# Kernel optimization log

Hardware: AMD Instinct MI355X
Metric: run time of the kernel (lower is better)

The kernel has to match this reference:

```python
import jax, jax.numpy as jnp
import numpy as np

SR = 16000
N_FFT = 1024
HOP = 256
WIN = 1024
N_MELS = 80
EPS = 1e-8
DRY_W, RIR_W = 3.0, 1.0
TIME_W, FREQ_W, MEL_W = 1.0, 0.5, 0.3
CONSIST_W, RIR_REG_W = 0.2, 0.1


def _hann(n):
    # torch.hann_window(periodic=True)
    return (0.5 - 0.5 * jnp.cos(2.0 * jnp.pi * jnp.arange(n) / n)).astype(jnp.float32)


def _stft(x):
    """torchaudio.transforms.Spectrogram(power=None, normalized=True) equivalent.
    x: [..., T] -> complex [..., n_freqs, n_frames]"""
    shp = x.shape
    T = shp[-1]
    xf = x.reshape(-1, T)
    pad = N_FFT // 2
    xp = jnp.pad(xf, ((0, 0), (pad, pad)), mode='reflect')  # center=True
    n_frames = 1 + T // HOP
    idx = jnp.arange(n_frames)[:, None] * HOP + jnp.arange(N_FFT)[None, :]
    win = _hann(WIN)
    frames = xp[:, idx] * win[None, None, :]              # [N, frames, n_fft]
    spec = jnp.fft.rfft(frames, axis=-1)                  # [N, frames, freqs]
    spec = spec / jnp.sqrt(jnp.sum(win ** 2))             # normalized='window'
    return spec.reshape(shp[:-1] + (n_frames, N_FFT // 2 + 1)).swapaxes(-1, -2)


def _mel_fb():
    # torchaudio melscale_fbanks, htk scale, norm=None, f_min=0, f_max=sr/2
    n_freqs = N_FFT // 2 + 1
    all_freqs = np.linspace(0.0, SR / 2.0, n_freqs)
    hz2mel = lambda f: 2595.0 * np.log10(1.0 + f / 700.0)
    mel2hz = lambda m: 700.0 * (10.0 ** (m / 2595.0) - 1.0)
    m_pts = np.linspace(hz2mel(0.0), hz2mel(SR / 2.0), N_MELS + 2)
    f_pts = mel2hz(m_pts)
    f_diff = f_pts[1:] - f_pts[:-1]
    slopes = f_pts[None, :] - all_freqs[:, None]
    down = -slopes[:, :-2] / f_diff[:-1]
    up = slopes[:, 2:] / f_diff[1:]
    fb = np.maximum(0.0, np.minimum(down, up))
    return jnp.asarray(fb, jnp.float32)  # [n_freqs, n_mels]

_FB = _mel_fb()


def _l1(a, b):
    return jnp.mean(jnp.abs(a - b))


def _freq_loss(pred, target):
    ps, ts = _stft(pred), _stft(target)
    mag_loss = _l1(jnp.abs(ps), jnp.abs(ts))
    dphi = jnp.angle(ps) - jnp.angle(ts)
    # cosine sim of unit [cos, sin] vectors == cos(delta phase)
    phase_loss = 1.0 - jnp.mean(jnp.cos(dphi))
    return mag_loss + 0.1 * phase_loss


def _mel_loss(pred, target):
    pm = jnp.einsum('...ft,fm->...mt', jnp.abs(_stft(pred)) ** 2, _FB)
    tm = jnp.einsum('...ft,fm->...mt', jnp.abs(_stft(target)) ** 2, _FB)
    return _l1(jnp.log(pm + EPS), jnp.log(tm + EPS))


def _consistency_loss(pred_dry, pred_rir, mix):
    # full linear convolution along time, truncated to first T samples
    T = pred_dry.shape[-1]
    n = 2 * T
    D = jnp.fft.rfft(pred_dry, n=n, axis=-1)
    R = jnp.fft.rfft(pred_rir, n=n, axis=-1)
    rec = jnp.fft.irfft(D * R, n=n, axis=-1)[..., :T]
    return _l1(rec, mix[..., :T])


def _rir_reg_loss(pred_rir):
    T = pred_rir.shape[-1]
    sparsity = jnp.mean(jnp.abs(pred_rir))
    seg = T // 4
    decay = 0.0
    for i in range(3):
        e1 = jnp.mean(pred_rir[:, :, i * seg:(i + 1) * seg] ** 2)
        e2 = jnp.mean(pred_rir[:, :, (i + 1) * seg:(i + 2) * seg] ** 2)
        decay = decay + jax.nn.relu(e2 - 0.8 * e1)
    return sparsity + decay


def setup_inputs() -> dict:
    key = jax.random.key(0)
    ks = jax.random.split(key, 5)
    shape = (32, 2, 64000)
    names = ['pred_dry', 'pred_rir', 'target_dry', 'target_rir', 'mix']
    return {n: jax.random.normal(k, shape, dtype=jnp.float32) for n, k in zip(names, ks)}


def reference(pred_dry, pred_rir, target_dry, target_rir, mix):
    dry_time = _l1(pred_dry, target_dry)
    dry_freq = _freq_loss(pred_dry, target_dry)
    dry_mel = _mel_loss(pred_dry, target_dry)
    total_dry = TIME_W * dry_time + FREQ_W * dry_freq + MEL_W * dry_mel

    rir_time = _l1(pred_rir, target_rir)
    rir_reg = _rir_reg_loss(pred_rir)
    total_rir = rir_time + RIR_REG_W * rir_reg

    consist = _consistency_loss(pred_dry, pred_rir, mix)
    total = DRY_W * total_dry + RIR_W * total_rir + CONSIST_W * consist
    return total
```

## Files before the change

### kernel.cpp

```cpp
#include <hip/hip_runtime.h>
#include <math.h>

#define ROWS 64
#define TLEN 64000
#define NFR 251
#define NMELS 80
#define NFB 131072
#define PI2F 6.28318530717958647692f
#define PI_F 3.14159265358979323846f

__device__ double g_part[64][12];

__device__ constexpr int DR[16] = {0,4,8,12,1,5,9,13,2,6,10,14,3,7,11,15};
__device__ constexpr int RM[16] = {0,3,2,1,15,14,13,12,11,10,9,8,7,6,5,4};

__device__ inline int dr4(int i){ return ((i & 3) << 2) | (i >> 2); }
__device__ inline int SW(int k){ return k + (k >> 5); }

__device__ inline void atomAddD(double* p, double v){
  __hip_atomic_fetch_add(p, v, __ATOMIC_RELAXED, __HIP_MEMORY_SCOPE_AGENT);
}
__device__ inline int brev6(int x){ return (int)((unsigned)__brev((unsigned)x) >> 26); }
__device__ inline float2 cmul(float2 a, float2 b){
  return make_float2(a.x*b.x - a.y*b.y, a.x*b.y + a.y*b.x);
}
__device__ inline float wred(float v){
#pragma unroll
  for (int o = 32; o > 0; o >>= 1) v += __shfl_down(v, o, 64);
  return v;
}

__device__ inline void wave_fence(){
  asm volatile("s_waitcnt lgkmcnt(0)" ::: "memory");
}

template<int S, int N>
__device__ inline void fft64_lanes(float2* v, int l){
  float2 W[5];
#pragma unroll
  for (int si = 0; si < 5; ++si){
    int d = 32 >> si;
    float a = (float)S * PI_F * (float)(l & (d-1)) * (1.0f/(float)d);
    float sn, cs; __sincosf(a, &sn, &cs);
    W[si] = make_float2(cs, sn);
  }
#pragma unroll
  for (int si = 0; si < 6; ++si){
    int d = 32 >> si;
    bool hi = (l & d) != 0;
#pragma unroll
    for (int rr = 0; rr < N; ++rr){
      float2 x = v[rr];
      float tx = __shfl_xor(x.x, d, 64);
      float ty = __shfl_xor(x.y, d, 64);
      float sx = x.x + tx, sy = x.y + ty;
      float dx = tx - x.x, dy = ty - x.y;
      float rx, ry;
      if (si < 5){ rx = dx*W[si].x - dy*W[si].y; ry = dx*W[si].y + dy*W[si].x; }
      else       { rx = dx; ry = dy; }
      v[rr].x = hi ? rx : sx;
      v[rr].y = hi ? ry : sy;
    }
  }
}

template<int S>
__device__ inline void fft16_reg(float2* v){
  const float Sf = (float)S;
  const float C1 = 0.9238795325112867f, S1 = 0.3826834323650898f, C2 = 0.7071067811865476f;
  const float2 W1[4] = {{1.f,0.f},{C1,Sf*S1},{C2,Sf*C2},{S1,Sf*C1}};
  const float2 W2[4] = {{1.f,0.f},{C2,Sf*C2},{0.f,Sf},{-C2,Sf*C2}};
  const float2 W3[4] = {{1.f,0.f},{S1,Sf*C1},{-C2,Sf*C2},{-C1,-Sf*S1}};
#pragma unroll
  for (int j = 0; j < 4; ++j){
    float2 x0=v[j], x1=v[j+4], x2=v[j+8], x3=v[j+12];
    float2 t0={x0.x+x2.x, x0.y+x2.y}, t1={x0.x-x2.x, x0.y-x2.y};
    float2 t2={x1.x+x3.x, x1.y+x3.y}, t3={x1.x-x3.x, x1.y-x3.y};
    float2 y0={t0.x+t2.x, t0.y+t2.y};
    float2 y2={t0.x-t2.x, t0.y-t2.y};
    float2 y1={t1.x - Sf*t3.y, t1.y + Sf*t3.x};
    float2 y3={t1.x + Sf*t3.y, t1.y - Sf*t3.x};
    v[j]=y0; v[j+4]=cmul(y1,W1[j]); v[j+8]=cmul(y2,W2[j]); v[j+12]=cmul(y3,W3[j]);
  }
#pragma unroll
  for (int b = 0; b < 4; ++b){
    float2 x0=v[4*b], x1=v[4*b+1], x2=v[4*b+2], x3=v[4*b+3];
    float2 t0={x0.x+x2.x, x0.y+x2.y}, t1={x0.x-x2.x, x0.y-x2.y};
    float2 t2={x1.x+x3.x, x1.y+x3.y}, t3={x1.x-x3.x, x1.y-x3.y};
    v[4*b]   = make_float2(t0.x+t2.x, t0.y+t2.y);
    v[4*b+2] = make_float2(t0.x-t2.x, t0.y-t2.y);
    v[4*b+1] = make_float2(t1.x - Sf*t3.y, t1.y + Sf*t3.x);
    v[4*b+3] = make_float2(t1.x + Sf*t3.y, t1.y - Sf*t3.x);
  }
}

template<int S>
__device__ inline void fft128_wave(float2* v, int l){
  float2 a = {v[0].x+v[1].x, v[0].y+v[1].y};
  float2 b = {v[0].x-v[1].x, v[0].y-v[1].y};
  float ang = (float)S * PI_F * (float)l * (1.0f/64.0f);
  float sn, cs; __sincosf(ang, &sn, &cs);
  v[0] = a; v[1] = cmul(b, make_float2(cs, sn));
  fft64_lanes<S,2>(v, l);
}

template<int S>
__device__ inline void fft8p(float2* y){
  const float Sf = (float)S;
  const float C2 = 0.7071067811865476f;
  float2 t0={y[0].x+y[4].x, y[0].y+y[4].y};
  float2 t1={y[1].x+y[5].x, y[1].y+y[5].y};
  float2 t2={y[2].x+y[6].x, y[2].y+y[6].y};
  float2 t3={y[3].x+y[7].x, y[3].y+y[7].y};
  float2 u0={y[0].x-y[4].x, y[0].y-y[4].y};
  float2 u1={y[1].x-y[5].x, y[1].y-y[5].y};
  float2 u2={y[2].x-y[6].x, y[2].y-y[6].y};
  float2 u3={y[3].x-y[7].x, y[3].y-y[7].y};
  { float x=u1.x, yy=u1.y; u1.x = C2*(x - Sf*yy); u1.y = C2*(Sf*x + yy); }
  { float x=u2.x, yy=u2.y; u2.x = -Sf*yy;         u2.y = Sf*x; }
  { float x=u3.x, yy=u3.y; u3.x = -C2*(x + Sf*yy); u3.y = C2*(Sf*x - yy); }
  {
    float2 e0={t0.x+t2.x,t0.y+t2.y}, e1={t0.x-t2.x,t0.y-t2.y};
    float2 o0={t1.x+t3.x,t1.y+t3.y}, o1={t1.x-t3.x,t1.y-t3.y};
    y[0]=make_float2(e0.x+o0.x, e0.y+o0.y);
    y[4]=make_float2(e0.x-o0.x, e0.y-o0.y);
    y[2]=make_float2(e1.x - Sf*o1.y, e1.y + Sf*o1.x);
    y[6]=make_float2(e1.x + Sf*o1.y, e1.y - Sf*o1.x);
  }
  {
    float2 e0={u0.x+u2.x,u0.y+u2.y}, e1={u0.x-u2.x,u0.y-u2.y};
    float2 o0={u1.x+u3.x,u1.y+u3.y}, o1={u1.x-u3.x,u1.y-u3.y};
    y[1]=make_float2(e0.x+o0.x, e0.y+o0.y);
    y[5]=make_float2(e0.x-o0.x, e0.y-o0.y);
    y[3]=make_float2(e1.x - Sf*o1.y, e1.y + Sf*o1.x);
    y[7]=make_float2(e1.x + Sf*o1.y, e1.y - Sf*o1.x);
  }
}

template<int S>
__device__ inline void fft64_lds(float2* v, int l, float2* scr){
  int s = l >> 3, a = l & 7;
  int sw = (s & 1);
#pragma unroll
  for (int h = 0; h < 2; ++h){
    float2* vh = v + 8*h;
#pragma unroll
    for (int r = 0; r < 8; ++r) scr[r*64 + l] = vh[r];
    wave_fence();
    float2 y[8];
#pragma unroll
    for (int j = 0; j < 8; ++j)
      y[j] = scr[s*64 + a + 8*((j + s) & 7)];
    fft8p<S>(y);
    {
      float ang = (float)S * PI2F * (float)l * (1.0f/64.0f);
      float sn, cs; __sincosf(ang, &sn, &cs);
      float2 b1 = make_float2(cs, sn), cur = b1;
#pragma unroll
      for (int c = 1; c < 8; ++c){
        y[c] = cmul(y[c], cur);
        if (c < 7) cur = cmul(cur, b1);
      }
    }
    wave_fence();
#pragma unroll
    for (int c = 0; c < 8; ++c)
      scr[s*64 + a + 8*(c ^ sw)] = y[c];
    wave_fence();
    float2 z[8];
#pragma unroll
    for (int j = 0; j < 8; ++j)
      z[j] = scr[s*64 + ((j + s) & 7) + 8*(a ^ sw)];
    fft8p<S>(z);
    {
      float ang2 = (float)S * PI2F * (float)s * 0.125f;
      float sn2, cs2; __sincosf(ang2, &sn2, &cs2);
      float2 b2 = make_float2(cs2, sn2), cur = b2;
#pragma unroll
      for (int d = 1; d < 8; ++d){
        z[d] = cmul(z[d], cur);
        if (d < 7) cur = cmul(cur, b2);
      }
    }
    wave_fence();
#pragma unroll
    for (int d = 0; d < 8; ++d)
      scr[s*64 + a + 8*(d ^ sw)] = z[d];
    wave_fence();
#pragma unroll
    for (int r = 0; r < 8; ++r)
      vh[r] = scr[r*64 + (l ^ ((r & 1) << 3))];
    wave_fence();
  }
}

template<int S>
__device__ inline void fft1024_lds(float2* v, int l, float2* scr){
  fft16_reg<S>(v);
  float a = (float)S * PI2F * (float)l * (1.0f/1024.0f);
  float sn, cs; __sincosf(a, &sn, &cs);
  float2 T = make_float2(cs, sn);
  float2 cur = T;
#pragma unroll
  for (int k2 = 1; k2 < 16; ++k2){
    v[DR[k2]] = cmul(v[DR[k2]], cur);
    if (k2 < 15) cur = cmul(cur, T);
  }
  fft64_lds<S>(v, l, scr);
}

__device__ inline void r4p(float2* v, int i0, int i1, int i2, int i3){
  float2 x0=v[i0], x1=v[i1], x2=v[i2], x3=v[i3];
  float2 t0={x0.x+x2.x, x0.y+x2.y}, t1={x0.x-x2.x, x0.y-x2.y};
  float2 t2={x1.x+x3.x, x1.y+x3.y}, t3={x1.x-x3.x, x1.y-x3.y};
  v[i0] = make_float2(t0.x+t2.x, t0.y+t2.y);
  v[i2] = make_float2(t0.x-t2.x, t0.y-t2.y);
  v[i1] = make_float2(t1.x - t3.y, t1.y + t3.x);
  v[i3] = make_float2(t1.x + t3.y, t1.y - t3.x);
}

__device__ inline void ifft16_reg(float2* v){
#pragma unroll
  for (int b = 0; b < 4; ++b) r4p(v, 4*b, 4*b+1, 4*b+2, 4*b+3);
  const float C1 = 0.9238795325112867f, S1 = 0.3826834323650898f, C2 = 0.7071067811865476f;
  const float2 W1[4] = {{1.f,0.f},{C1,S1},{C2,C2},{S1,C1}};
  const float2 W2[4] = {{1.f,0.f},{C2,C2},{0.f,1.f},{-C2,C2}};
  const float2 W3[4] = {{1.f,0.f},{S1,C1},{-C2,C2},{-C1,-S1}};
#pragma unroll
  for (int j = 1; j < 4; ++j){
    v[j+4]  = cmul(v[j+4],  W1[j]);
    v[j+8]  = cmul(v[j+8],  W2[j]);
    v[j+12] = cmul(v[j+12], W3[j]);
  }
#pragma unroll
  for (int j = 0; j < 4; ++j) r4p(v, j, j+4, j+8, j+12);
}

__device__ inline void ifft1024_lds(float2* v, int l, float2* scr){
  fft64_lds<1>(v, l, scr);
  float a = PI2F * (float)l * (1.0f/1024.0f);
  float sn, cs; __sincosf(a, &sn, &cs);
  float2 T = make_float2(cs, sn);
  float2 cur = T;
#pragma unroll
  for (int k2 = 1; k2 < 16; ++k2){
    v[DR[k2]] = cmul(v[DR[k2]], cur);
    if (k2 < 15) cur = cmul(cur, T);
  }
  ifft16_reg(v);
}

template<int N>
__device__ inline void ifft64_lanes(float2* v, int l){
  float2 W[5];
#pragma unroll
  for (int si = 0; si < 5; ++si){
    int d = 32 >> si;
    float a = PI_F * (float)(l & (d-1)) * (1.0f/(float)d);
    float sn, cs; __sincosf(a, &sn, &cs);
    W[si] = make_float2(cs, sn);
  }
#pragma unroll
  for (int si = 5; si >= 0; --si){
    int d = 32 >> si;
    bool hi = (l & d) != 0;
#pragma unroll
    for (int rr = 0; rr < N; ++rr){
      float2 x = v[rr];
      float2 xp = x;
      if (si < 5 && hi) xp = cmul(x, W[si]);
      float tx = __shfl_xor(xp.x, d, 64);
      float ty = __shfl_xor(xp.y, d, 64);
      v[rr].x = hi ? (tx - xp.x) : (xp.x + tx);
      v[rr].y = hi ? (ty - xp.y) : (xp.y + ty);
    }
  }
}

__device__ inline void ifft128_wave(float2* v, int l){
  ifft64_lanes<2>(v, l);
  float ang = PI_F * (float)l * (1.0f/64.0f);
  float sn, cs; __sincosf(ang, &sn, &cs);
  v[1] = cmul(v[1], make_float2(cs, sn));
  float2 a = {v[0].x+v[1].x, v[0].y+v[1].y};
  float2 b = {v[0].x-v[1].x, v[0].y-v[1].y};
  v[0] = a; v[1] = b;
}

extern "C" __global__ void __launch_bounds__(256) k_init(){
  int t = blockIdx.x*256 + threadIdx.x;
  if (t < 768) ((double*)g_part)[t] = 0.0;
}

extern "C" __global__ void __launch_bounds__(256) k_time(
    const float* __restrict__ pd, const float* __restrict__ td,
    const float* __restrict__ pr, const float* __restrict__ tr){
  const int N4 = ROWS*TLEN/4;
  int stride = gridDim.x * 256;
  float sdt=0.f, srt=0.f, ssp=0.f, e0=0.f, e1=0.f, e2=0.f, e3=0.f;
  const float4* pd4 = (const float4*)pd;
  const float4* td4 = (const float4*)td;
  const float4* pr4 = (const float4*)pr;
  const float4* tr4 = (const float4*)tr;
  for (int i = blockIdx.x*256 + threadIdx.x; i < N4; i += stride){
    float4 a = pd4[i], b = td4[i], p = pr4[i], q = tr4[i];
    sdt += fabsf(a.x-b.x)+fabsf(a.y-b.y)+fabsf(a.z-b.z)+fabsf(a.w-b.w);
    srt += fabsf(p.x-q.x)+fabsf(p.y-q.y)+fabsf(p.z-q.z)+fabsf(p.w-q.w);
    ssp += fabsf(p.x)+fabsf(p.y)+fabsf(p.z)+fabsf(p.w);
    float p2 = p.x*p.x + p.y*p.y + p.z*p.z + p.w*p.w;
    int seg = (i % 16000) / 4000;
    if (seg == 0) e0 += p2; else if (seg == 1) e1 += p2;
    else if (seg == 2) e2 += p2; else e3 += p2;
  }
  sdt = wred(sdt); srt = wred(srt); ssp = wred(ssp);
  e0 = wred(e0); e1 = wred(e1); e2 = wred(e2); e3 = wred(e3);
  if ((threadIdx.x & 63) == 0){
    int bank = (blockIdx.x*4 + (threadIdx.x >> 6)) & 63;
    atomAddD(&g_part[bank][0], (double)sdt);
    atomAddD(&g_part[bank][1], (double)srt);
    atomAddD(&g_part[bank][2], (double)ssp);
    atomAddD(&g_part[bank][3], (double)e0);
    atomAddD(&g_part[bank][4], (double)e1);
    atomAddD(&g_part[bank][5], (double)e2);
    atomAddD(&g_part[bank][6], (double)e3);
  }
}

extern "C" __global__ void __launch_bounds__(64) k_stft(
    const float* __restrict__ pd, const float* __restrict__ td){
  __shared__ float2 scr[512];
  __shared__ float2 spec0[64];
  __shared__ float2 pt[530];
  int l = threadIdx.x;
  int frame = (blockIdx.x & 7) * (ROWS*NFR/8) + (blockIdx.x >> 3);
  int r = frame / NFR, fr = frame - r*NFR;
  const float* pdr = pd + (size_t)r*TLEN;
  const float* tdr = td + (size_t)r*TLEN;
  const float scale = 0.05103103630798288f;
  int base = fr*256 - 512;
  float2 v[16];
#pragma unroll
  for (int m = 0; m < 16; ++m){
    int j = l + 64*m;
    int g = base + j;
    g = (g < 0) ? -g : ((g >= TLEN) ? (2*TLEN - 2 - g) : g);
    float w = (0.5f - 0.5f*__cosf((PI2F/1024.0f)*(float)j)) * scale;
    v[m] = make_float2(pdr[g]*w, tdr[g]*w);
  }
  fft1024_lds<-1>(v, l, scr);
  spec0[l] = v[0];
  float magp = 0.f, cosp = 0.f;
#pragma unroll
  for (int rr = 1; rr < 16; ++rr){
    float2 z = v[rr];
    float2 zm;
    zm.x = __shfl_xor(v[RM[rr]].x, 63, 64);
    zm.y = __shfl_xor(v[RM[rr]].y, 63, 64);
    int k = DR[rr] + 16*l;
    float px = 0.5f*(z.x + zm.x), py = 0.5f*(z.y - zm.y);
    float tx = 0.5f*(z.y + zm.y), ty = -0.5f*(z.x - zm.x);
    float ppk = px*px + py*py, ttk = tx*tx + ty*ty;
    float rp = rsqrtf(fmaxf(ppk, 1e-30f)), rt = rsqrtf(fmaxf(ttk, 1e-30f));
    magp += 0.5f*fabsf(ppk*rp - ttk*rt);
    cosp += 0.5f*((px*tx + py*ty)*rp*rt);
    int kk = (k <= 512) ? k : 1024 - k;
    pt[SW(kk)] = make_float2(ppk, ttk);
  }
  if (l <= 32){
    float2 z  = spec0[l];
    float2 zm = spec0[(64 - l) & 63];
    float px = 0.5f*(z.x + zm.x), py = 0.5f*(z.y - zm.y);
    float tx = 0.5f*(z.y + zm.y), ty = -0.5f*(z.x - zm.x);
    float ppk = px*px + py*py, ttk = tx*tx + ty*ty;
    float rp = rsqrtf(fmaxf(ppk, 1e-30f)), rt = rsqrtf(fmaxf(ttk, 1e-30f));
    magp += fabsf(ppk*rp - ttk*rt);
    cosp += (px*tx + py*ty)*rp*rt;
    pt[SW(16*l)] = make_float2(ppk, ttk);
  }
  float melp = 0.f;
  const float C = (2595.0f * log10f(1.0f + 8000.0f/700.0f))
                  * (1.0f/81.0f) * (1.0f/2595.0f) * 2.302585093f;
  const float df = 15.625f;
  {
    int m = l;
    float f0 = 700.0f*(__expf(C*(float)(m  )) - 1.0f);
    float f1 = 700.0f*(__expf(C*(float)(m+1)) - 1.0f);
    float f2 = 700.0f*(__expf(C*(float)(m+2)) - 1.0f);
    float i1 = 1.0f/(f1 - f0), i2 = 1.0f/(f2 - f1);
    int lo = (int)ceilf(f0 * (1.0f/df));  if (lo < 0) lo = 0;
    int hi = (int)floorf(f2 * (1.0f/df)); if (hi > 512) hi = 512;
    float pm = 0.f, tm = 0.f;
#pragma unroll 2
    for (int k = lo; k <= hi; ++k){
      float frq = df*(float)k;
      float c = fmaxf(fminf((frq - f0)*i1, (f2 - frq)*i2), 0.f);
      float2 w = pt[SW(k)];
      pm += c*w.x; tm += c*w.y;
    }
    melp += fabsf(__logf(pm + 1e-8f) - __logf(tm + 1e-8f));
  }
  {
    int m = 64 + (l >> 2), q = l & 3;
    float f0 = 700.0f*(__expf(C*(float)(m  )) - 1.0f);
    float f1 = 700.0f*(__expf(C*(float)(m+1)) - 1.0f);
    float f2 = 700.0f*(__expf(C*(float)(m+2)) - 1.0f);
    float i1 = 1.0f/(f1 - f0), i2 = 1.0f/(f2 - f1);
    int lo = (int)ceilf(f0 * (1.0f/df));  if (lo < 0) lo = 0;
    int hi = (int)floorf(f2 * (1.0f/df)); if (hi > 512) hi = 512;
    int n = hi - lo + 1;
    int ch = (n + 3) >> 2;
    int k0 = lo + q*ch;
    int k1 = k0 + ch; if (k1 > hi + 1) k1 = hi + 1;
    float pm = 0.f, tm = 0.f;
#pragma unroll 2
    for (int k = k0; k < k1; ++k){
      float frq = df*(float)k;
      float c = fmaxf(fminf((frq - f0)*i1, (f2 - frq)*i2), 0.f);
      float2 w = pt[SW(k)];
      pm += c*w.x; tm += c*w.y;
    }
    pm += __shfl_xor(pm, 1, 64); pm += __shfl_xor(pm, 2, 64);
    tm += __shfl_xor(tm, 1, 64); tm += __shfl_xor(tm, 2, 64);
    if (q == 0)
      melp += fabsf(__logf(pm + 1e-8f) - __logf(tm + 1e-8f));
  }
  magp = wred(magp); cosp = wred(cosp); melp = wred(melp);
  if (l == 0){
    int bank = blockIdx.x & 63;
    atomAddD(&g_part[bank][7], (double)magp);
    atomAddD(&g_part[bank][8], (double)cosp);
    atomAddD(&g_part[bank][9], (double)melp);
  }
}

extern "C" __global__ void __launch_bounds__(256) k_fwd1(
    const float* __restrict__ pd, const float* __restrict__ pr,
    float2* __restrict__ buf, int row0){
  __shared__ float SM[6144];
  float* LA = SM;
  float* LB = SM + 3000;
  float2* LT = (float2*)SM;
  int wid = threadIdx.x >> 6, l = threadIdx.x & 63;
  int tid = threadIdx.x;
  float2* scr = (float2*)SM + (size_t)wid*512;
  int flat = blockIdx.x;
  int cpx = gridDim.x >> 3;
  int w = (flat & 7) * cpx + (flat >> 3);
  int rl = w >> 5;
  int n1base = (w & 31) * 4;
  int n1 = n1base + wid;
  const float* a = pd + (size_t)(row0+rl)*TLEN;
  const float* b = pr + (size_t)(row0+rl)*TLEN;
  for (int i = tid; i < 1000; i += 256){
    int n2 = i >> 1, wp = (i & 1)*2;
    float2 va = *(const float2*)&a[n1base + wp + 128*n2];
    float2 vb = *(const float2*)&b[n1base + wp + 128*n2];
    *(float2*)&LA[n2*6 + wp] = va;
    *(float2*)&LB[n2*6 + wp] = vb;
  }
  __syncthreads();
  float2 v[16];
#pragma unroll
  for (int m = 0; m < 16; ++m){
    int n2 = l + 64*m;
    if (n2 < 500) v[m] = make_float2(LA[n2*6 + wid], LB[n2*6 + wid]);
    else          v[m] = make_float2(0.f, 0.f);
  }
  __syncthreads();
  fft1024_lds<-1>(v, l, scr);
  const float tw = -(PI2F / (float)NFB);
#pragma unroll
  for (int rr = 0; rr < 16; ++rr){
    int K = DR[rr] + 16*l;
    float ang = tw * (float)(n1*K);
    float sn, cs; __sincosf(ang, &sn, &cs);
    v[rr] = cmul(v[rr], make_float2(cs, sn));
  }
  float2* rowp = buf + (size_t)rl*NFB;
  __syncthreads();
#pragma unroll
  for (int c = 0; c < 2; ++c){
#pragma unroll
    for (int rrl = 0; rrl < 8; ++rrl)
      LT[wid*513 + rrl*64 + l] = v[c*8 + rrl];
    __syncthreads();
#pragma unroll
    for (int it = 0; it < 4; ++it){
      int idx = tid + it*256;
      int s = idx >> 1, nw = (idx & 1)*2;
      float2 x = LT[nw*513 + s], y = LT[(nw+1)*513 + s];
      *(float4*)&rowp[(size_t)(c*512 + s)*128 + n1base + nw] =
          make_float4(x.x, x.y, y.x, y.y);
    }
    __syncthreads();
  }
}

__device__ inline float2 pointmul(float2 z, float2 zm){
  float Dx = 0.5f*(z.x + zm.x), Dy = 0.5f*(z.y - zm.y);
  float Rx = 0.5f*(z.y + zm.y), Ry = -0.5f*(z.x - zm.x);
  return make_float2(Dx*Rx - Dy*Ry, Dx*Ry + Dy*Rx);
}

extern "C" __global__ void __launch_bounds__(256) k_mid(float2* __restrict__ buf){
  int wid = threadIdx.x >> 6, l = threadIdx.x & 63;
  int p = blockIdx.x*4 + wid;
  if (p > 512) return;
  int k2A = p, k2B = (1024 - p) & 1023;
  int sA = dr4(k2A & 15)*64 + (k2A >> 4);
  int sB = dr4(k2B & 15)*64 + (k2B >> 4);
  float2* base = buf + (size_t)blockIdx.y*NFB;
  float2* rA = base + (size_t)sA*128;
  float2* rB = base + (size_t)sB*128;
  bool pair = (sB != sA);
  float2 vA[2] = { rA[l], rA[l+64] };
  float2 vB[2];
  if (pair){ vB[0] = rB[l]; vB[1] = rB[l+64]; }
  fft128_wave<-1>(vA, l);
  if (pair) fft128_wave<-1>(vB, l);
  float2 cA[2];
  if (p == 0){
    int kb = brev6(l);
    int q0 = brev6((64 - kb) & 63);
    float2 zm0 = { __shfl(vA[0].x, q0, 64), __shfl(vA[0].y, q0, 64) };
    float2 zm1 = { __shfl_xor(vA[1].x, 63, 64), __shfl_xor(vA[1].y, 63, 64) };
    cA[0] = pointmul(vA[0], zm0);
    cA[1] = pointmul(vA[1], zm1);
  } else {
    const float2* src = pair ? vB : vA;
    float2 zm0 = { __shfl_xor(src[1].x, 63, 64), __shfl_xor(src[1].y, 63, 64) };
    float2 zm1 = { __shfl_xor(src[0].x, 63, 64), __shfl_xor(src[0].y, 63, 64) };
    cA[0] = pointmul(vA[0], zm0);
    cA[1] = pointmul(vA[1], zm1);
  }
  const float twi = PI2F / (float)NFB;
  ifft128_wave(cA, l);
#pragma unroll
  for (int rr = 0; rr < 2; ++rr){
    int n1 = l + 64*rr;
    float ang = twi * (float)(n1*k2A);
    float sn, cs; __sincosf(ang, &sn, &cs);
    float2 val = cmul(cA[rr], make_float2(cs, sn));
    rA[n1] = val;
    if (pair) rB[n1] = make_float2(val.x, -val.y);
  }
}

extern "C" __global__ void __launch_bounds__(128) k_inv2(
    const float* __restrict__ mix, float2* __restrict__ buf, int row0){
  __shared__ float SM[5052];
  float2* LT = (float2*)SM;
  float* LM = SM + 2052;
  int wid = threadIdx.x >> 6, l = threadIdx.x & 63;
  int tid = threadIdx.x;
  float2* scr = (float2*)SM + (size_t)wid*512;
  int flat = blockIdx.x;
  int cpx = gridDim.x >> 3;
  int w = (flat & 7) * cpx + (flat >> 3);
  int rl = w >> 5;
  int n1base = (w & 31) * 4;
  float2* rowp = buf + (size_t)rl*NFB;
  float2 v[16];
#pragma unroll
  for (int c = 0; c < 2; ++c){
#pragma unroll
    for (int it = 0; it < 8; ++it){
      int idx = tid + it*128;
      int s = idx >> 1, nw = (idx & 1)*2;
      float4 q = *(const float4*)&rowp[(size_t)(c*512 + s)*128 + n1base + nw];
      LT[(nw >> 1)*513 + s] = make_float2(q.x - q.w, q.y + q.z);
    }
    __syncthreads();
#pragma unroll
    for (int rrl = 0; rrl < 8; ++rrl)
      v[c*8 + rrl] = LT[wid*513 + rrl*64 + l];
    __syncthreads();
  }
  const float* mr = mix + (size_t)(row0+rl)*TLEN;
  for (int i = tid; i < 1000; i += 128){
    int n2 = i >> 1, wp = (i & 1)*2;
    *(float2*)&LM[n2*6 + wp] = *(const float2*)&mr[n1base + wp + 128*n2];
  }
  ifft1024_lds(v, l, scr);
  __syncthreads();
  const float invn = 1.0f/(float)NFB;
  float acc = 0.f;
#pragma unroll
  for (int m = 0; m < 16; ++m){
    int n2 = l + 64*m;
    if (n2 < 500){
      float2 mm = *(const float2*)&LM[n2*6 + 2*wid];
      acc += fabsf(v[m].x*invn - mm.x) + fabsf(v[m].y*invn - mm.y);
    }
  }
  acc = wred(acc);
  if (l == 0){
    int bank = (flat*2 + wid) & 63;
    atomAddD(&g_part[bank][10], (double)acc);
  }
}

extern "C" __global__ void __launch_bounds__(64) k_finalize(float* __restrict__ out){
  __shared__ double s[12];
  int t = threadIdx.x;
  if (t < 12){
    double v = 0.0;
    for (int b = 0; b < 64; ++b) v += g_part[b][t];
    s[t] = v;
  }
  __syncthreads();
  if (t == 0){
    double dt = s[0] / 4096000.0;
    double rt = s[1] / 4096000.0;
    double sp = s[2] / 4096000.0;
    double e0 = s[3] / 1024000.0, e1 = s[4] / 1024000.0;
    double e2 = s[5] / 1024000.0, e3 = s[6] / 1024000.0;
    double dec = fmax(e1 - 0.8*e0, 0.0) + fmax(e2 - 0.8*e1, 0.0) + fmax(e3 - 0.8*e2, 0.0);
    double c1 = 8240832.0;
    double freq = s[7]/c1 + 0.1*(1.0 - s[8]/c1);
    double mel  = s[9] / 1285120.0;
    double cons = s[10] / 4096000.0;
    double total = 3.0*(dt + 0.5*freq + 0.3*mel)
                 + (rt + 0.1*(sp + dec))
                 + 0.2*cons;
    out[0] = (float)total;
  }
}

extern "C" void kernel_launch(void* const* d_in, const int* in_sizes, int n_in,
                              void* d_out, int out_size, void* d_ws, size_t ws_size,
                              hipStream_t stream){
  const float* pd = (const float*)d_in[0];
  const float* pr = (const float*)d_in[1];
  const float* td = (const float*)d_in[2];
  const float* tr = (const float*)d_in[3];
  const float* mx = (const float*)d_in[4];
  float* out = (float*)d_out;
  float2* buf = (float2*)d_ws;

  size_t rowBytes = (size_t)NFB * sizeof(float2);
  int maxrows = (int)(ws_size / rowBytes);
  if (maxrows > ROWS) maxrows = ROWS;
  if (maxrows < 1) maxrows = 1;
  int chrows = 1;
  const int cand[7] = {64, 32, 16, 8, 4, 2, 1};
  for (int i = 0; i < 7; ++i) if (cand[i] <= maxrows){ chrows = cand[i]; break; }

  hipLaunchKernelGGL(k_init, dim3(3), dim3(256), 0, stream);
  hipLaunchKernelGGL(k_time, dim3(2048), dim3(256), 0, stream, pd, td, pr, tr);
  hipLaunchKernelGGL(k_stft, dim3(ROWS*NFR), dim3(64), 0, stream, pd, td);
  for (int row0 = 0; row0 < ROWS; row0 += chrows){
    int nr = ROWS - row0; if (nr > chrows) nr = chrows;
    hipLaunchKernelGGL(k_fwd1, dim3(32*nr),   dim3(256), 0, stream, pd, pr, buf, row0);
    hipLaunchKernelGGL(k_mid,  dim3(129, nr), dim3(256), 0, stream, buf);
    hipLaunchKernelGGL(k_inv2, dim3(32*nr),   dim3(128), 0, stream, mx, buf, row0);
  }
  hipLaunchKernelGGL(k_finalize, dim3(1), dim3(64), 0, stream, out);
}
```

Before: 254.5 us.

## Batch four k2 columns per wave in k_mid with LDS FFT64, drop mirrored writes

k_mid now has each wave handle four frequency pairs at once, using the LDS-based radix-8 FFT64 instead of per-column shuffle butterflies, and the grid shrinks from 129 to 33 blocks per row. Only the primary column is written back. k_inv2 reconstructs the mirrored half on the fly by reading the conjugate-symmetric source row. The aim is to cut shuffle-heavy work and halve the write traffic in the middle stage, at the cost of more registers, extra LDS and scattered reads in k_inv2.

```diff
diff --git a/kernel.cpp b/kernel.cpp
--- a/kernel.cpp
+++ b/kernel.cpp
@@ -32,36 +32,6 @@
 
 __device__ inline void wave_fence(){
   asm volatile("s_waitcnt lgkmcnt(0)" ::: "memory");
-}
-
-template<int S, int N>
-__device__ inline void fft64_lanes(float2* v, int l){
-  float2 W[5];
-#pragma unroll
-  for (int si = 0; si < 5; ++si){
-    int d = 32 >> si;
-    float a = (float)S * PI_F * (float)(l & (d-1)) * (1.0f/(float)d);
-    float sn, cs; __sincosf(a, &sn, &cs);
-    W[si] = make_float2(cs, sn);
-  }
-#pragma unroll
-  for (int si = 0; si < 6; ++si){
-    int d = 32 >> si;
-    bool hi = (l & d) != 0;
-#pragma unroll
-    for (int rr = 0; rr < N; ++rr){
-      float2 x = v[rr];
-      float tx = __shfl_xor(x.x, d, 64);
-      float ty = __shfl_xor(x.y, d, 64);
-      float sx = x.x + tx, sy = x.y + ty;
-      float dx = tx - x.x, dy = ty - x.y;
-      float rx, ry;
-      if (si < 5){ rx = dx*W[si].x - dy*W[si].y; ry = dx*W[si].y + dy*W[si].x; }
-      else       { rx = dx; ry = dy; }
-      v[rr].x = hi ? rx : sx;
-      v[rr].y = hi ? ry : sy;
-    }
-  }
 }
 
 template<int S>
@@ -92,16 +62,6 @@
     v[4*b+1] = make_float2(t1.x - Sf*t3.y, t1.y + Sf*t3.x);
     v[4*b+3] = make_float2(t1.x + Sf*t3.y, t1.y - Sf*t3.x);
   }
-}
-
-template<int S>
-__device__ inline void fft128_wave(float2* v, int l){
-  float2 a = {v[0].x+v[1].x, v[0].y+v[1].y};
-  float2 b = {v[0].x-v[1].x, v[0].y-v[1].y};
-  float ang = (float)S * PI_F * (float)l * (1.0f/64.0f);
-  float sn, cs; __sincosf(ang, &sn, &cs);
-  v[0] = a; v[1] = cmul(b, make_float2(cs, sn));
-  fft64_lanes<S,2>(v, l);
 }
 
 template<int S>
@@ -137,12 +97,12 @@
   }
 }
 
-template<int S>
-__device__ inline void fft64_lds(float2* v, int l, float2* scr){
+template<int S, int NS>
+__device__ inline void fft64_ldsn(float2* v, int l, float2* scr){
   int s = l >> 3, a = l & 7;
   int sw = (s & 1);
 #pragma unroll
-  for (int h = 0; h < 2; ++h){
+  for (int h = 0; h < NS/8; ++h){
     float2* vh = v + 8*h;
 #pragma unroll
     for (int r = 0; r < 8; ++r) scr[r*64 + l] = vh[r];
@@ -206,7 +166,7 @@
     v[DR[k2]] = cmul(v[DR[k2]], cur);
     if (k2 < 15) cur = cmul(cur, T);
   }
-  fft64_lds<S>(v, l, scr);
+  fft64_ldsn<S,16>(v, l, scr);
 }
 
 __device__ inline void r4p(float2* v, int i0, int i1, int i2, int i3){
@@ -237,7 +197,7 @@
 }
 
 __device__ inline void ifft1024_lds(float2* v, int l, float2* scr){
-  fft64_lds<1>(v, l, scr);
+  fft64_ldsn<1,16>(v, l, scr);
   float a = PI2F * (float)l * (1.0f/1024.0f);
   float sn, cs; __sincosf(a, &sn, &cs);
   float2 T = make_float2(cs, sn);
@@ -248,43 +208,6 @@
     if (k2 < 15) cur = cmul(cur, T);
   }
   ifft16_reg(v);
-}
-
-template<int N>
-__device__ inline void ifft64_lanes(float2* v, int l){
-  float2 W[5];
-#pragma unroll
-  for (int si = 0; si < 5; ++si){
-    int d = 32 >> si;
-    float a = PI_F * (float)(l & (d-1)) * (1.0f/(float)d);
-    float sn, cs; __sincosf(a, &sn, &cs);
-    W[si] = make_float2(cs, sn);
-  }
-#pragma unroll
-  for (int si = 5; si >= 0; --si){
-    int d = 32 >> si;
-    bool hi = (l & d) != 0;
-#pragma unroll
-    for (int rr = 0; rr < N; ++rr){
-      float2 x = v[rr];
-      float2 xp = x;
-      if (si < 5 && hi) xp = cmul(x, W[si]);
-      float tx = __shfl_xor(xp.x, d, 64);
-      float ty = __shfl_xor(xp.y, d, 64);
-      v[rr].x = hi ? (tx - xp.x) : (xp.x + tx);
-      v[rr].y = hi ? (ty - xp.y) : (xp.y + ty);
-    }
-  }
-}
-
-__device__ inline void ifft128_wave(float2* v, int l){
-  ifft64_lanes<2>(v, l);
-  float ang = PI_F * (float)l * (1.0f/64.0f);
-  float sn, cs; __sincosf(ang, &sn, &cs);
-  v[1] = cmul(v[1], make_float2(cs, sn));
-  float2 a = {v[0].x+v[1].x, v[0].y+v[1].y};
-  float2 b = {v[0].x-v[1].x, v[0].y-v[1].y};
-  v[0] = a; v[1] = b;
 }
 
 extern "C" __global__ void __launch_bounds__(256) k_init(){
@@ -503,46 +426,86 @@
 }
 
 extern "C" __global__ void __launch_bounds__(256) k_mid(float2* __restrict__ buf){
+  __shared__ float2 SCR[2048];
   int wid = threadIdx.x >> 6, l = threadIdx.x & 63;
-  int p = blockIdx.x*4 + wid;
-  if (p > 512) return;
-  int k2A = p, k2B = (1024 - p) & 1023;
-  int sA = dr4(k2A & 15)*64 + (k2A >> 4);
-  int sB = dr4(k2B & 15)*64 + (k2B >> 4);
+  float2* scr = SCR + (size_t)wid*512;
   float2* base = buf + (size_t)blockIdx.y*NFB;
-  float2* rA = base + (size_t)sA*128;
-  float2* rB = base + (size_t)sB*128;
-  bool pair = (sB != sA);
-  float2 vA[2] = { rA[l], rA[l+64] };
-  float2 vB[2];
-  if (pair){ vB[0] = rB[l]; vB[1] = rB[l+64]; }
-  fft128_wave<-1>(vA, l);
-  if (pair) fft128_wave<-1>(vB, l);
-  float2 cA[2];
-  if (p == 0){
-    int kb = brev6(l);
-    int q0 = brev6((64 - kb) & 63);
-    float2 zm0 = { __shfl(vA[0].x, q0, 64), __shfl(vA[0].y, q0, 64) };
-    float2 zm1 = { __shfl_xor(vA[1].x, 63, 64), __shfl_xor(vA[1].y, 63, 64) };
-    cA[0] = pointmul(vA[0], zm0);
-    cA[1] = pointmul(vA[1], zm1);
-  } else {
-    const float2* src = pair ? vB : vA;
-    float2 zm0 = { __shfl_xor(src[1].x, 63, 64), __shfl_xor(src[1].y, 63, 64) };
-    float2 zm1 = { __shfl_xor(src[0].x, 63, 64), __shfl_xor(src[0].y, 63, 64) };
-    cA[0] = pointmul(vA[0], zm0);
-    cA[1] = pointmul(vA[1], zm1);
-  }
-  const float twi = PI2F / (float)NFB;
-  ifft128_wave(cA, l);
-#pragma unroll
-  for (int rr = 0; rr < 2; ++rr){
-    int n1 = l + 64*rr;
-    float ang = twi * (float)(n1*k2A);
+  int p0 = (blockIdx.x*4 + wid)*4;
+  float2 v[16];
+  int sAr[4];
+#pragma unroll
+  for (int j = 0; j < 4; ++j){
+    int p = p0 + j;
+    bool ok = (p <= 512);
+    int k2A = ok ? p : 0;
+    int k2B = (1024 - k2A) & 1023;
+    int sA = dr4(k2A & 15)*64 + (k2A >> 4);
+    int sB = dr4(k2B & 15)*64 + (k2B >> 4);
+    sAr[j] = sA;
+    if (ok){
+      const float2* rA = base + (size_t)sA*128;
+      v[4*j+0] = rA[l]; v[4*j+1] = rA[l+64];
+      if (sB != sA){
+        const float2* rB = base + (size_t)sB*128;
+        v[4*j+2] = rB[l]; v[4*j+3] = rB[l+64];
+      } else {
+        v[4*j+2] = make_float2(0.f,0.f); v[4*j+3] = make_float2(0.f,0.f);
+      }
+    } else {
+      v[4*j+0]=v[4*j+1]=v[4*j+2]=v[4*j+3]=make_float2(0.f,0.f);
+    }
+  }
+  {
+    float ang = -PI_F * (float)l * (1.0f/64.0f);
     float sn, cs; __sincosf(ang, &sn, &cs);
-    float2 val = cmul(cA[rr], make_float2(cs, sn));
-    rA[n1] = val;
-    if (pair) rB[n1] = make_float2(val.x, -val.y);
+    float2 W = make_float2(cs, sn);
+#pragma unroll
+    for (int i = 0; i < 8; ++i){
+      float2 x0 = v[2*i], x1 = v[2*i+1];
+      float2 aa = {x0.x+x1.x, x0.y+x1.y};
+      float2 bb = {x0.x-x1.x, x0.y-x1.y};
+      v[2*i] = aa; v[2*i+1] = cmul(bb, W);
+    }
+  }
+  fft64_ldsn<-1,16>(v, l, scr);
+  float2 ci[8];
+#pragma unroll
+  for (int j = 0; j < 4; ++j){
+    int p = p0 + j;
+    float2 zm0, zm1;
+    if (p == 0){
+      int q0 = (64 - l) & 63;
+      zm0.x = __shfl(v[0].x, q0, 64); zm0.y = __shfl(v[0].y, q0, 64);
+      zm1.x = __shfl_xor(v[1].x, 63, 64); zm1.y = __shfl_xor(v[1].y, 63, 64);
+    } else if (p == 512){
+      zm0.x = __shfl_xor(v[4*j+1].x, 63, 64); zm0.y = __shfl_xor(v[4*j+1].y, 63, 64);
+      zm1.x = __shfl_xor(v[4*j+0].x, 63, 64); zm1.y = __shfl_xor(v[4*j+0].y, 63, 64);
+    } else {
+      zm0.x = __shfl_xor(v[4*j+3].x, 63, 64); zm0.y = __shfl_xor(v[4*j+3].y, 63, 64);
+      zm1.x = __shfl_xor(v[4*j+2].x, 63, 64); zm1.y = __shfl_xor(v[4*j+2].y, 63, 64);
+    }
+    ci[2*j]   = pointmul(v[4*j+0], zm0);
+    ci[2*j+1] = pointmul(v[4*j+1], zm1);
+  }
+  fft64_ldsn<1,8>(ci, l, scr);
+  {
+    float angw = PI_F * (float)l * (1.0f/64.0f);
+    float snw, csw; __sincosf(angw, &snw, &csw);
+    float2 W = make_float2(csw, snw);
+    const float twi = PI2F / (float)NFB;
+#pragma unroll
+    for (int j = 0; j < 4; ++j){
+      int p = p0 + j;
+      if (p > 512) continue;
+      float2 E = ci[2*j], O = cmul(ci[2*j+1], W);
+      float2 o0 = {E.x+O.x, E.y+O.y};
+      float2 o1 = {E.x-O.x, E.y-O.y};
+      float2* rA = base + (size_t)sAr[j]*128;
+      { float ang = twi * (float)(l*p); float sn, cs; __sincosf(ang, &sn, &cs);
+        rA[l] = cmul(o0, make_float2(cs, sn)); }
+      { float ang = twi * (float)((l+64)*p); float sn, cs; __sincosf(ang, &sn, &cs);
+        rA[l+64] = cmul(o1, make_float2(cs, sn)); }
+    }
   }
 }
 
@@ -567,8 +530,16 @@
     for (int it = 0; it < 8; ++it){
       int idx = tid + it*128;
       int s = idx >> 1, nw = (idx & 1)*2;
-      float4 q = *(const float4*)&rowp[(size_t)(c*512 + s)*128 + n1base + nw];
-      LT[(nw >> 1)*513 + s] = make_float2(q.x - q.w, q.y + q.z);
+      int srow = c*512 + s;
+      int rr = srow >> 6, lr = srow & 63;
+      int d = dr4(rr);
+      int K = d + 16*lr;
+      bool mir = (K > 512);
+      int srcrow = mir ? (dr4((16 - d) & 15)*64 + (64 - lr - (d > 0 ? 1 : 0)))
+                       : srow;
+      float4 q = *(const float4*)&rowp[(size_t)srcrow*128 + n1base + nw];
+      LT[(nw >> 1)*513 + s] = mir ? make_float2(q.x + q.w, q.z - q.y)
+                                  : make_float2(q.x - q.w, q.y + q.z);
     }
     __syncthreads();
 #pragma unroll
@@ -651,9 +622,9 @@
   hipLaunchKernelGGL(k_stft, dim3(ROWS*NFR), dim3(64), 0, stream, pd, td);
   for (int row0 = 0; row0 < ROWS; row0 += chrows){
     int nr = ROWS - row0; if (nr > chrows) nr = chrows;
-    hipLaunchKernelGGL(k_fwd1, dim3(32*nr),   dim3(256), 0, stream, pd, pr, buf, row0);
-    hipLaunchKernelGGL(k_mid,  dim3(129, nr), dim3(256), 0, stream, buf);
-    hipLaunchKernelGGL(k_inv2, dim3(32*nr),   dim3(128), 0, stream, mx, buf, row0);
+    hipLaunchKernelGGL(k_fwd1, dim3(32*nr),  dim3(256), 0, stream, pd, pr, buf, row0);
+    hipLaunchKernelGGL(k_mid,  dim3(33, nr), dim3(256), 0, stream, buf);
+    hipLaunchKernelGGL(k_inv2, dim3(32*nr),  dim3(128), 0, stream, mx, buf, row0);
   }
   hipLaunchKernelGGL(k_finalize, dim3(1), dim3(64), 0, stream, out);
 }
```

Measured after the change: 252.1 us. Within noise of the previous version (-0.9%).
